# Optimization experiments

Measured on AMD Instinct MI355X. Metric: run time of the kernel, lower is better.

The kernel has to match this reference:

```python
import jax, jax.numpy as jnp
import numpy as np

N_NODES = 50000
N_EDGES = 800000
D_FEAT = 32
J = 4
NUM_GRAPHS = 64
MAX_SCALE = 2 ** (J - 1)  # 8 diffusion steps


def _propagate(x, src, dst, w):
    # gather x_j, weight per-edge, scatter-add into target nodes
    msgs = x[src] * w[:, None]
    return jax.ops.segment_sum(msgs, dst, num_segments=N_NODES)


def _diffuse(x, src, dst, w):
    outs = []
    x_curr = x
    for step in range(1, MAX_SCALE + 1):
        x_curr = _propagate(x_curr, src, dst, w)
        if step & (step - 1) == 0:  # collect at powers of two: 1,2,4,8 -> J scales
            outs.append(x_curr)
    return outs


def setup_inputs() -> dict:
    key = jax.random.key(0)
    k1, k2, k3, k4 = jax.random.split(key, 4)
    X = jax.random.normal(k1, (N_NODES, D_FEAT), dtype=jnp.float32)
    edge_index = jax.random.randint(k2, (2, N_EDGES), 0, N_NODES, dtype=jnp.int64)
    edge_weight = jax.random.uniform(k3, (N_EDGES,), dtype=jnp.float32)
    batch = jnp.sort(jax.random.randint(k4, (N_NODES,), 0, NUM_GRAPHS, dtype=jnp.int64))
    return {"X": X, "edge_index": edge_index, "edge_weight": edge_weight, "batch": batch}


def reference(X, edge_index, edge_weight, batch):
    src, dst = edge_index[0], edge_index[1]
    diff_list = _diffuse(X, src, dst, edge_weight)
    # F0: deepest scale
    F0 = diff_list[-1]
    # F1: first-order wavelet coefficients |psi_j x|
    F1 = jnp.concatenate(
        [jnp.abs(diff_list[i - 1] - diff_list[i]) for i in range(1, len(diff_list))],
        axis=1,
    )
    # F2: second-order, diffuse concatenated scales once more
    U = jnp.concatenate(diff_list, axis=1)  # [N, J*d]
    U_diff = _diffuse(U, src, dst, edge_weight)
    res = []
    for j in range(J):
        cs, ce = j * D_FEAT, (j + 1) * D_FEAT
        for jp in range(j + 1, J):
            res.append(jnp.abs(U_diff[jp][:, cs:ce] - U_diff[jp - 1][:, cs:ce]))
    F2 = jnp.concatenate(res, axis=1)
    feats = jnp.concatenate([F0, F1, F2], axis=1)  # [N, d*(1 + (J-1) + J*(J-1)/2)] = [N, 320]
    # global_mean_pool over batch assignment
    sums = jax.ops.segment_sum(feats, batch, num_segments=NUM_GRAPHS)
    counts = jax.ops.segment_sum(jnp.ones((feats.shape[0],), feats.dtype), batch, num_segments=NUM_GRAPHS)
    return sums / jnp.maximum(counts, 1.0)[:, None]
```

## Files before the change

kernel.cpp:

```cpp
#include <hip/hip_runtime.h>

#define N_NODES 50000
#define N_EDGES 800000
#define D_FEAT 32
#define NUM_GRAPHS 64
#define FEATS 320
#define NBIN 128
#define BINSH 9
#define CE 4096
#define NCHUNK ((N_EDGES + CE - 1) / CE)
#define NPB ((N_NODES + 511) / 512)

__device__ __forceinline__ unsigned short f2bf(float f) {
    unsigned int u = __float_as_uint(f);
    u = (u + 0x7fffu + ((u >> 16) & 1u)) >> 16;
    return (unsigned short)u;
}
__device__ __forceinline__ float bf2f(unsigned short h) {
    return __uint_as_float((unsigned int)h << 16);
}


__global__ void binA_kernel(const int* __restrict__ dst, int* __restrict__ counts, int n) {
    __shared__ int h[NBIN];
    int t = threadIdx.x;
    if (t < NBIN) h[t] = 0;
    __syncthreads();
    int s0 = blockIdx.x * CE, e0 = min(s0 + CE, n);
    for (int i = s0 + t; i < e0; i += blockDim.x)
        atomicAdd(&h[dst[i] >> BINSH], 1);
    __syncthreads();
    if (t < NBIN) counts[blockIdx.x * NBIN + t] = h[t];
}

__global__ void binB_kernel(int* __restrict__ counts, int* __restrict__ binBase) {
    __shared__ int s[NBIN];
    int b = threadIdx.x;
    int tot = 0;
    #pragma unroll 8
    for (int c = 0; c < NCHUNK; ++c) tot += counts[c * NBIN + b];
    s[b] = tot;
    __syncthreads();
    for (int off = 1; off < NBIN; off <<= 1) {
        int u = (b >= off) ? s[b - off] : 0;
        __syncthreads();
        s[b] += u;
        __syncthreads();
    }
    int base = s[b] - tot;
    binBase[b] = base;
    if (b == NBIN - 1) binBase[NBIN] = s[b];
    int running = base;
    #pragma unroll 4
    for (int c = 0; c < NCHUNK; ++c) {
        int idx = c * NBIN + b;
        int v = counts[idx];
        counts[idx] = running;
        running += v;
    }
}

__global__ __launch_bounds__(256) void binC_kernel(const int* __restrict__ src,
                                                   const int* __restrict__ dst,
                                                   const float* __restrict__ w,
                                                   const int* __restrict__ counts,
                                                   int2* __restrict__ tmp, int n) {
    __shared__ int h[NBIN], sc[NBIN], cur[NBIN], gbase[NBIN];
    __shared__ int2 srec[CE];
    __shared__ unsigned char sbin[CE];
    int t = threadIdx.x;
    if (t < NBIN) h[t] = 0;
    __syncthreads();
    int s0 = blockIdx.x * CE, e0 = min(s0 + CE, n);
    int cnt = e0 - s0;
    for (int i = s0 + t; i < e0; i += blockDim.x)
        atomicAdd(&h[dst[i] >> BINSH], 1);
    __syncthreads();
    if (t < NBIN) sc[t] = h[t];
    __syncthreads();
    for (int off = 1; off < NBIN; off <<= 1) {
        int u = (t < NBIN && t >= off) ? sc[t - off] : 0;
        __syncthreads();
        if (t < NBIN) sc[t] += u;
        __syncthreads();
    }
    if (t < NBIN) {
        cur[t] = 0;
        gbase[t] = counts[blockIdx.x * NBIN + t];
    }
    __syncthreads();
    for (int i = s0 + t; i < e0; i += blockDim.x) {
        int d = dst[i];
        int b = d >> BINSH;
        int pos = (sc[b] - h[b]) + atomicAdd(&cur[b], 1);
        srec[pos] = make_int2(src[i] | ((int)f2bf(w[i]) << 16), d & 511);
        sbin[pos] = (unsigned char)b;
    }
    __syncthreads();
    for (int j = t; j < cnt; j += blockDim.x) {
        int b = sbin[j];
        tmp[gbase[b] + (j - (sc[b] - h[b]))] = srec[j];
    }
}

__global__ __launch_bounds__(256) void place_kernel(const int* __restrict__ binBase,
                                                    const int2* __restrict__ tmp,
                                                    unsigned int* __restrict__ edges,
                                                    int* __restrict__ rowptr, int n) {
    __shared__ int h[512], sc[512], cur[512];
    int b = blockIdx.x;
    int t = threadIdx.x;
    int base = binBase[b], end = binBase[b + 1];
    for (int i = t; i < 512; i += 256) { h[i] = 0; cur[i] = 0; }
    __syncthreads();
    for (int e = base + t; e < end; e += 256)
        atomicAdd(&h[tmp[e].y], 1);
    __syncthreads();
    for (int i = t; i < 512; i += 256) sc[i] = h[i];
    __syncthreads();
    for (int off = 1; off < 512; off <<= 1) {
        int i0 = t, i1 = t + 256;
        int a0 = (i0 >= off) ? sc[i0 - off] : 0;
        int a1 = (i1 >= off) ? sc[i1 - off] : 0;
        __syncthreads();
        sc[i0] += a0;
        sc[i1] += a1;
        __syncthreads();
    }
    int node0 = b << BINSH;
    for (int i = t; i < 512; i += 256) {
        int node = node0 + i;
        if (node <= n) rowptr[node] = base + sc[i] - h[i];
    }
    if (b == 0 && t == 0) rowptr[0] = 0;
    __syncthreads();
    for (int e = base + t; e < end; e += 256) {
        int2 p = tmp[e];
        int loc = p.y;
        int pos = base + (sc[loc] - h[loc]) + atomicAdd(&cur[loc], 1);
        edges[pos] = (unsigned int)p.x;
    }
}


__global__ void cvt_kernel(const float4* __restrict__ xin, ushort4* __restrict__ xout, int n4) {
    int i = blockIdx.x * blockDim.x + threadIdx.x;
    if (i < n4) {
        float4 v = xin[i];
        ushort4 o;
        o.x = f2bf(v.x); o.y = f2bf(v.y); o.z = f2bf(v.z); o.w = f2bf(v.w);
        xout[i] = o;
    }
}


__global__ void gbound_kernel(const int* __restrict__ batch, int* __restrict__ gstart, int n) {
    int i = blockIdx.x * blockDim.x + threadIdx.x;
    if (i >= n) return;
    int g = batch[i];
    int gp = (i == 0) ? -1 : batch[i - 1];
    for (int gg = gp + 1; gg <= g; ++gg) gstart[gg] = i;
    if (i == n - 1)
        for (int gg = g + 1; gg <= NUM_GRAPHS; ++gg) gstart[gg] = n;
}


__global__ __launch_bounds__(256) void spmm_kernel(const ushort4* __restrict__ xin,
                                                   ushort4* __restrict__ yout,
                                                   const int* __restrict__ rowptr,
                                                   const unsigned int* __restrict__ edges,
                                                   int n) {
    int lane = threadIdx.x & 7;
    int node = (blockIdx.x * blockDim.x + threadIdx.x) >> 3;
    if (node >= n) return;
    int e0 = rowptr[node], e1 = rowptr[node + 1];
    float a0 = 0.f, a1 = 0.f, a2 = 0.f, a3 = 0.f;
    int e = e0;
    int e8 = e0 + ((e1 - e0) & ~7);
    for (; e < e8; e += 8) {
        unsigned int r[8];
        #pragma unroll
        for (int u = 0; u < 8; ++u) r[u] = edges[e + u];
        ushort4 v[8];
        #pragma unroll
        for (int u = 0; u < 8; ++u)
            v[u] = xin[(size_t)(r[u] & 0xffff) * 8 + lane];
        #pragma unroll
        for (int u = 0; u < 8; ++u) {
            float w = bf2f((unsigned short)(r[u] >> 16));
            a0 += bf2f(v[u].x) * w;
            a1 += bf2f(v[u].y) * w;
            a2 += bf2f(v[u].z) * w;
            a3 += bf2f(v[u].w) * w;
        }
    }
    for (; e < e1; ++e) {
        unsigned int r = edges[e];
        ushort4 v = xin[(size_t)(r & 0xffff) * 8 + lane];
        float w = bf2f((unsigned short)(r >> 16));
        a0 += bf2f(v.x) * w; a1 += bf2f(v.y) * w; a2 += bf2f(v.z) * w; a3 += bf2f(v.w) * w;
    }
    yout[(size_t)node * 8 + lane] = make_ushort4(f2bf(a0), f2bf(a1), f2bf(a2), f2bf(a3));
}


struct PoolArgs10 {
    const unsigned short* P[10];
    const unsigned short* Q[10];
};

__global__ __launch_bounds__(320) void pool_kernel(PoolArgs10 a, const int* __restrict__ gstart,
                                                   float* __restrict__ out) {
    int k = threadIdx.x >> 5;
    int f = threadIdx.x & 31;
    int g = blockIdx.x >> 4;
    int s = blockIdx.x & 15;
    int gs = gstart[g], ge = gstart[g + 1];
    int len = ge - gs;
    int i0 = gs + ((len * s) >> 4);
    int i1 = gs + ((len * (s + 1)) >> 4);
    const unsigned short* __restrict__ P = a.P[k];
    const unsigned short* __restrict__ Q = a.Q[k];
    float acc = 0.f;
    if (Q) {
        for (int i = i0; i < i1; ++i)
            acc += fabsf(bf2f(P[(size_t)i * 32 + f]) - bf2f(Q[(size_t)i * 32 + f]));
    } else {
        for (int i = i0; i < i1; ++i)
            acc += bf2f(P[(size_t)i * 32 + f]);
    }
    if (i1 > i0) atomicAdd(&out[g * FEATS + k * 32 + f], acc);
}

__global__ void divide_kernel(float* __restrict__ out, const int* __restrict__ gstart, int total) {
    int i = blockIdx.x * blockDim.x + threadIdx.x;
    if (i < total) {
        int g = i / FEATS;
        float c = (float)(gstart[g + 1] - gstart[g]);
        out[i] /= fmaxf(c, 1.0f);
    }
}


extern "C" void kernel_launch(void* const* d_in, const int* in_sizes, int n_in,
                              void* d_out, int out_size, void* d_ws, size_t ws_size,
                              hipStream_t stream) {
    const float* X     = (const float*)d_in[0];
    const int*   ei    = (const int*)d_in[1];
    const float* ew    = (const float*)d_in[2];
    const int*   batch = (const int*)d_in[3];
    float* out = (float*)d_out;

    const int N = N_NODES, E = N_EDGES;
    const int* src = ei;
    const int* dst = ei + E;

    char* base = (char*)d_ws;
    size_t off = 0;
    auto alloc = [&](size_t bytes) -> void* {
        void* p = base + off;
        off += (bytes + 255) & ~(size_t)255;
        return p;
    };
    unsigned short* y[13];
    for (int k = 0; k <= 12; ++k) y[k] = (unsigned short*)alloc((size_t)N * 32 * 2);

    int*  rowptr  = (int*)alloc((size_t)(N + 4) * 4);
    int*  gstart  = (int*)alloc((NUM_GRAPHS + 1) * 4);
    int*  counts  = (int*)alloc((size_t)NCHUNK * NBIN * 4);
    int*  binBase = (int*)alloc((NBIN + 1) * 4);
    int2* tmp     = (int2*)alloc((size_t)E * 8);
    unsigned int* edges = (unsigned int*)alloc((size_t)E * 4);

    hipMemsetAsync(out, 0, (size_t)out_size * 4, stream);

    binA_kernel<<<NCHUNK, 256, 0, stream>>>(dst, counts, E);
    binB_kernel<<<1, NBIN, 0, stream>>>(counts, binBase);
    binC_kernel<<<NCHUNK, 256, 0, stream>>>(src, dst, ew, counts, tmp, E);
    place_kernel<<<NPB, 256, 0, stream>>>(binBase, tmp, edges, rowptr, N);

    cvt_kernel<<<(N * 32 / 4 + 255) / 256, 256, 0, stream>>>((const float4*)X, (ushort4*)y[0],
                                                             N * 32 / 4);
    gbound_kernel<<<(N + 255) / 256, 256, 0, stream>>>(batch, gstart, N);

    const int SPMM_GRID = (N * 8 + 255) / 256;
    for (int k = 1; k <= 12; ++k) {
        spmm_kernel<<<SPMM_GRID, 256, 0, stream>>>((const ushort4*)y[k - 1], (ushort4*)y[k],
                                                   rowptr, edges, N);
    }

    {
        PoolArgs10 p{};
        const unsigned short* Ps[10] = {y[8], y[1], y[2], y[4], y[3], y[5], y[9], y[6], y[10], y[12]};
        const unsigned short* Qs[10] = {nullptr, y[2], y[4], y[8], y[2], y[3], y[5], y[4], y[6], y[8]};
        for (int k = 0; k < 10; ++k) { p.P[k] = Ps[k]; p.Q[k] = Qs[k]; }
        pool_kernel<<<NUM_GRAPHS * 16, 320, 0, stream>>>(p, gstart, out);
    }

    divide_kernel<<<(out_size + 255) / 256, 256, 0, stream>>>(out, gstart, out_size);
}
```

Before: 294.5 us.

## Split feature matrices into two 16-column halves to shrink SpMM gather working set

Node features are stored as two separate planes of 16 bf16 columns each instead of one interleaved 32-column row. Each SpMM block processes one half for 64 nodes, and consecutive blocks are arranged so that blocks covering the same half run together. The intent is to halve the random-gather working set so more of it stays in cache. The cost is that each edge list is read twice and the per-edge gathers become 32-byte segments. The conversion and pooling kernels are updated to match the new layout.

```diff
diff --git a/kernel.cpp b/kernel.cpp
--- a/kernel.cpp
+++ b/kernel.cpp
@@ -10,6 +10,8 @@
 #define CE 4096
 #define NCHUNK ((N_EDGES + CE - 1) / CE)
 #define NPB ((N_NODES + 511) / 512)
+#define HALF4 (N_NODES * 4)
+#define HALFS (N_NODES * 16)
 
 __device__ __forceinline__ unsigned short f2bf(float f) {
     unsigned int u = __float_as_uint(f);
@@ -143,14 +145,14 @@
 }
 
 
-__global__ void cvt_kernel(const float4* __restrict__ xin, ushort4* __restrict__ xout, int n4) {
+__global__ void cvt_kernel(const float4* __restrict__ xin, ushort4* __restrict__ xout, int n) {
     int i = blockIdx.x * blockDim.x + threadIdx.x;
-    if (i < n4) {
-        float4 v = xin[i];
-        ushort4 o;
-        o.x = f2bf(v.x); o.y = f2bf(v.y); o.z = f2bf(v.z); o.w = f2bf(v.w);
-        xout[i] = o;
-    }
+    if (i >= n * 8) return;
+    int node = i >> 3, q = i & 7;
+    float4 v = xin[i];
+    ushort4 o;
+    o.x = f2bf(v.x); o.y = f2bf(v.y); o.z = f2bf(v.z); o.w = f2bf(v.w);
+    xout[(size_t)(q >> 2) * HALF4 + (size_t)node * 4 + (q & 3)] = o;
 }
 
 
@@ -170,9 +172,13 @@
                                                    const int* __restrict__ rowptr,
                                                    const unsigned int* __restrict__ edges,
                                                    int n) {
-    int lane = threadIdx.x & 7;
-    int node = (blockIdx.x * blockDim.x + threadIdx.x) >> 3;
+    int c = blockIdx.x & 7;
+    int half = c >> 2;
+    int sub = ((blockIdx.x >> 3) << 2) + (c & 3);
+    int lane = threadIdx.x & 3;
+    int node = sub * 64 + (threadIdx.x >> 2);
     if (node >= n) return;
+    const ushort4* __restrict__ xh = xin + (size_t)half * HALF4;
     int e0 = rowptr[node], e1 = rowptr[node + 1];
     float a0 = 0.f, a1 = 0.f, a2 = 0.f, a3 = 0.f;
     int e = e0;
@@ -184,7 +190,7 @@
         ushort4 v[8];
         #pragma unroll
         for (int u = 0; u < 8; ++u)
-            v[u] = xin[(size_t)(r[u] & 0xffff) * 8 + lane];
+            v[u] = xh[(size_t)(r[u] & 0xffff) * 4 + lane];
         #pragma unroll
         for (int u = 0; u < 8; ++u) {
             float w = bf2f((unsigned short)(r[u] >> 16));
@@ -196,11 +202,12 @@
     }
     for (; e < e1; ++e) {
         unsigned int r = edges[e];
-        ushort4 v = xin[(size_t)(r & 0xffff) * 8 + lane];
+        ushort4 v = xh[(size_t)(r & 0xffff) * 4 + lane];
         float w = bf2f((unsigned short)(r >> 16));
         a0 += bf2f(v.x) * w; a1 += bf2f(v.y) * w; a2 += bf2f(v.z) * w; a3 += bf2f(v.w) * w;
     }
-    yout[(size_t)node * 8 + lane] = make_ushort4(f2bf(a0), f2bf(a1), f2bf(a2), f2bf(a3));
+    yout[(size_t)half * HALF4 + (size_t)node * 4 + lane] =
+        make_ushort4(f2bf(a0), f2bf(a1), f2bf(a2), f2bf(a3));
 }
 
 
@@ -219,15 +226,16 @@
     int len = ge - gs;
     int i0 = gs + ((len * s) >> 4);
     int i1 = gs + ((len * (s + 1)) >> 4);
-    const unsigned short* __restrict__ P = a.P[k];
-    const unsigned short* __restrict__ Q = a.Q[k];
+    size_t off = (size_t)(f >> 4) * HALFS + (f & 15);
+    const unsigned short* __restrict__ P = a.P[k] + off;
+    const unsigned short* __restrict__ Q = a.Q[k] ? (a.Q[k] + off) : nullptr;
     float acc = 0.f;
     if (Q) {
         for (int i = i0; i < i1; ++i)
-            acc += fabsf(bf2f(P[(size_t)i * 32 + f]) - bf2f(Q[(size_t)i * 32 + f]));
+            acc += fabsf(bf2f(P[(size_t)i * 16]) - bf2f(Q[(size_t)i * 16]));
     } else {
         for (int i = i0; i < i1; ++i)
-            acc += bf2f(P[(size_t)i * 32 + f]);
+            acc += bf2f(P[(size_t)i * 16]);
     }
     if (i1 > i0) atomicAdd(&out[g * FEATS + k * 32 + f], acc);
 }
@@ -279,11 +287,10 @@
     binC_kernel<<<NCHUNK, 256, 0, stream>>>(src, dst, ew, counts, tmp, E);
     place_kernel<<<NPB, 256, 0, stream>>>(binBase, tmp, edges, rowptr, N);
 
-    cvt_kernel<<<(N * 32 / 4 + 255) / 256, 256, 0, stream>>>((const float4*)X, (ushort4*)y[0],
-                                                             N * 32 / 4);
+    cvt_kernel<<<(N * 8 + 255) / 256, 256, 0, stream>>>((const float4*)X, (ushort4*)y[0], N);
     gbound_kernel<<<(N + 255) / 256, 256, 0, stream>>>(batch, gstart, N);
 
-    const int SPMM_GRID = (N * 8 + 255) / 256;
+    const int SPMM_GRID = 196 * 8;
     for (int k = 1; k <= 12; ++k) {
         spmm_kernel<<<SPMM_GRID, 256, 0, stream>>>((const ushort4*)y[k - 1], (ushort4*)y[k],
                                                    rowptr, edges, N);
```

Measured after the change: 306.2 us. 4.0% more time.
